# Optimization experiments

Hardware: AMD Instinct MI355X
Metric: run time of the kernel (lower is better)

## Reference

```python
import jax, jax.numpy as jnp
import numpy as np

N = 50000        # nodes
E = 800000       # edges (no self loops; GATv2Conv adds them itself)
F_IN = 256       # n_feats
DIM_H = 64       # hidden per head (layer 1)
HEADS = 4        # heads (layer 1)
N_CLASSES = 10
NEG_SLOPE = 0.2


def setup_inputs() -> dict:
    key = jax.random.key(0)
    ks = jax.random.split(key, 12)
    x = jax.random.normal(ks[0], (N, F_IN), dtype=jnp.float32)
    # edges with src != dst so PyG's remove_self_loops is a no-op
    src = jax.random.randint(ks[1], (E,), 0, N, dtype=jnp.int32)
    off = jax.random.randint(ks[2], (E,), 1, N, dtype=jnp.int32)
    dst = (src + off) % N
    edge_index = jnp.stack([src, dst], axis=0)  # [2, E]
    HC = HEADS * DIM_H
    s1 = 1.0 / np.sqrt(F_IN)
    s2 = 1.0 / np.sqrt(HC)
    W_l1 = jax.random.normal(ks[3], (F_IN, HC), dtype=jnp.float32) * s1
    W_r1 = jax.random.normal(ks[4], (F_IN, HC), dtype=jnp.float32) * s1
    att1 = jax.random.normal(ks[5], (HEADS, DIM_H), dtype=jnp.float32) * s2
    b1 = jnp.zeros((HC,), dtype=jnp.float32)
    W_l2 = jax.random.normal(ks[6], (HC, N_CLASSES), dtype=jnp.float32) * s2
    W_r2 = jax.random.normal(ks[7], (HC, N_CLASSES), dtype=jnp.float32) * s2
    att2 = jax.random.normal(ks[8], (1, N_CLASSES), dtype=jnp.float32) * (1.0 / np.sqrt(N_CLASSES))
    b2 = jnp.zeros((N_CLASSES,), dtype=jnp.float32)
    return {"x": x, "edge_index": edge_index,
            "W_l1": W_l1, "W_r1": W_r1, "att1": att1, "b1": b1,
            "W_l2": W_l2, "W_r2": W_r2, "att2": att2, "b2": b2}


def _gatv2_layer(x, src, dst, W_l, W_r, att, b, heads, ch):
    """One GATv2Conv layer (concat heads). src/dst already include self loops."""
    n = x.shape[0]
    xl = (x @ W_l).reshape(n, heads, ch)  # source transform (messages)
    xr = (x @ W_r).reshape(n, heads, ch)  # target transform
    # per-edge GATv2 score: att . LeakyReLU(x_l[src] + x_r[dst])
    e = jax.nn.leaky_relu(xl[src] + xr[dst], NEG_SLOPE)   # [E, H, C]
    score = jnp.einsum('ehc,hc->eh', e, att)              # [E, H]
    # segment softmax over incoming edges of each dst node
    m = jax.ops.segment_max(score, dst, num_segments=n)   # [N, H]
    ex = jnp.exp(score - m[dst])
    denom = jax.ops.segment_sum(ex, dst, num_segments=n)  # [N, H]
    alpha = ex / denom[dst]                               # [E, H]
    msg = xl[src] * alpha[:, :, None]                     # [E, H, C]
    out = jax.ops.segment_sum(msg, dst, num_segments=n)   # [N, H, C]
    return out.reshape(n, heads * ch) + b


def reference(x, edge_index, W_l1, W_r1, att1, b1, W_l2, W_r2, att2, b2):
    n = x.shape[0]
    loops = jnp.arange(n, dtype=edge_index.dtype)
    src = jnp.concatenate([edge_index[0], loops])  # add_self_loops=True
    dst = jnp.concatenate([edge_index[1], loops])
    h = _gatv2_layer(x, src, dst, W_l1, W_r1, att1, b1, HEADS, DIM_H)
    h = jax.nn.relu(h)
    out = _gatv2_layer(h, src, dst, W_l2, W_r2, att2, b2, 1, N_CLASSES)
    return out
```

## Files before the change

### kernel.cpp

```cpp
#include <hip/hip_runtime.h>
#include <hip/hip_bf16.h>

typedef unsigned short u16;
typedef unsigned int u32;
typedef short bf16x8 __attribute__((ext_vector_type(8)));
typedef float f32x4 __attribute__((ext_vector_type(4)));

constexpr int N_NODES = 50000;
constexpr int N_EDGES = 800000;
constexpr int ET      = N_EDGES + N_NODES;
constexpr int ETP     = ET + 3 * N_NODES;
constexpr int HC      = 256;
constexpr int NCLS    = 10;
constexpr float NEG   = 0.2f;
constexpr float LOG2E = 1.442695041f;

__device__ __forceinline__ u16 f2bf(float f) {
  u32 u = __float_as_uint(f);
  u += 0x7fffu + ((u >> 16) & 1u);
  return (u16)(u >> 16);
}
__device__ __forceinline__ float bf2f(u16 h) {
  return __uint_as_float(((u32)h) << 16);
}

__device__ __forceinline__ float dpp_ror8(float v) {
  return __uint_as_float(__builtin_amdgcn_mov_dpp(__float_as_uint(v), 0x128, 0xf, 0xf, true));
}
__device__ __forceinline__ float dpp_ror4(float v) {
  return __uint_as_float(__builtin_amdgcn_mov_dpp(__float_as_uint(v), 0x124, 0xf, 0xf, true));
}
__device__ __forceinline__ float dpp_ror2(float v) {
  return __uint_as_float(__builtin_amdgcn_mov_dpp(__float_as_uint(v), 0x122, 0xf, 0xf, true));
}
__device__ __forceinline__ float dpp_ror1(float v) {
  return __uint_as_float(__builtin_amdgcn_mov_dpp(__float_as_uint(v), 0x121, 0xf, 0xf, true));
}
__device__ __forceinline__ float row16_allsum(float p) {
  p += dpp_ror8(p);
  p += dpp_ror4(p);
  p += dpp_ror2(p);
  p += dpp_ror1(p);
  return p;
}


__global__ void k_hist(const int* __restrict__ ei, int* __restrict__ counts) {
  int e = blockIdx.x * 256 + threadIdx.x;
  if (e >= ET) return;
  int d = (e < N_EDGES) ? ei[N_EDGES + e] : (e - N_EDGES);
  atomicAdd(&counts[d], 1);
}

__global__ __launch_bounds__(256) void k_scan1(const int* __restrict__ counts,
                                               int* __restrict__ offsets,
                                               int* __restrict__ bsums) {
  __shared__ int sd[256];
  int t = threadIdx.x;
  int base = blockIdx.x * 1024 + t * 4;
  int v[4];
#pragma unroll
  for (int i = 0; i < 4; ++i) {
    int idx = base + i;
    v[i] = (idx < N_NODES) ? ((counts[idx] + 3) & ~3) : 0;
  }
  int tsum = v[0] + v[1] + v[2] + v[3];
  sd[t] = tsum;
  __syncthreads();
  for (int off = 1; off < 256; off <<= 1) {
    int x = (t >= off) ? sd[t - off] : 0;
    __syncthreads();
    sd[t] += x;
    __syncthreads();
  }
  int run = sd[t] - tsum;
#pragma unroll
  for (int i = 0; i < 4; ++i) {
    run += v[i];
    int idx = base + i;
    if (idx < N_NODES) offsets[idx + 1] = run;
  }
  if (t == 255) bsums[blockIdx.x] = sd[255];
}

__global__ __launch_bounds__(256) void k_scan2(int* __restrict__ bsums, int nb) {
  __shared__ int sd[256];
  int t = threadIdx.x;
  int v = (t < nb) ? bsums[t] : 0;
  sd[t] = v;
  __syncthreads();
  for (int off = 1; off < 256; off <<= 1) {
    int x = (t >= off) ? sd[t - off] : 0;
    __syncthreads();
    sd[t] += x;
    __syncthreads();
  }
  if (t < nb) bsums[t] = sd[t] - v;
}

__global__ void k_scan3(const int* __restrict__ bsums, int* __restrict__ offsets) {
  int i = blockIdx.x * 256 + threadIdx.x;
  if (i < N_NODES) offsets[i + 1] += bsums[i >> 10];
  if (i == 0) offsets[0] = 0;
}

__global__ void k_scatter(const int* __restrict__ ei, const int* __restrict__ offsets,
                          int* __restrict__ counts, int* __restrict__ srcs) {
  int e = blockIdx.x * 256 + threadIdx.x;
  if (e >= ET) return;
  int s, d;
  if (e < N_EDGES) { s = ei[e]; d = ei[N_EDGES + e]; }
  else             { s = e - N_EDGES; d = s; }
  int pos = offsets[d] + atomicSub(&counts[d], 1) - 1;
  srcs[pos] = s;
}

__global__ __launch_bounds__(256) void k_packW(const float* __restrict__ Wl,
                                               const float* __restrict__ Wr,
                                               u16* __restrict__ Wt_hi,
                                               u16* __restrict__ Wt_lo) {
  int c = blockIdx.x;
  int k = threadIdx.x;
  float w = (c < 256) ? Wl[k * 256 + c] : Wr[k * 256 + (c - 256)];
  u16 h = f2bf(w);
  float lo = w - bf2f(h);
  Wt_hi[c * 256 + k] = h;
  Wt_lo[c * 256 + k] = f2bf(lo);
}

__global__ __launch_bounds__(256) void k_gemm1_mfma(const float* __restrict__ x,
                                                    const u16* __restrict__ Wt_hi,
                                                    const u16* __restrict__ Wt_lo,
                                                    u16* __restrict__ xlb,
                                                    u16* __restrict__ xrb) {
  __shared__ char smem[61440];
  char* Ah = smem;
  char* Al = smem + 10240;
  char* Bh = smem + 20480;
  char* Bl = smem + 40960;

  int t = threadIdx.x;
  int lane = t & 63, wave = t >> 6;
  int wm = wave >> 1, wn = wave & 1;
  int row0 = blockIdx.x * 128;
  int bc = blockIdx.y;
  int col0 = bc * 256;

  f32x4 acc[4][8];
#pragma unroll
  for (int m = 0; m < 4; ++m)
#pragma unroll
    for (int n = 0; n < 8; ++n) acc[m][n] = (f32x4){0.f, 0.f, 0.f, 0.f};

  int ar = t >> 3;
  int ak4 = t & 7;
  int rr = lane & 15, kb = lane >> 4;

#pragma unroll 1
  for (int kk = 0; kk < 256; kk += 32) {
#pragma unroll
    for (int i = 0; i < 4; ++i) {
      int r = ar + 32 * i;
      int grow = row0 + r;
      if (grow >= N_NODES) grow = N_NODES - 1;
      float4 v = *(const float4*)&x[(size_t)grow * 256 + kk + ak4 * 4];
      u16 h0 = f2bf(v.x), h1 = f2bf(v.y), h2 = f2bf(v.z), h3 = f2bf(v.w);
      u16 l0 = f2bf(v.x - bf2f(h0)), l1 = f2bf(v.y - bf2f(h1));
      u16 l2 = f2bf(v.z - bf2f(h2)), l3 = f2bf(v.w - bf2f(h3));
      uint2 hp = make_uint2((u32)h0 | ((u32)h1 << 16), (u32)h2 | ((u32)h3 << 16));
      uint2 lp = make_uint2((u32)l0 | ((u32)l1 << 16), (u32)l2 | ((u32)l3 << 16));
      int boff = r * 80 + ak4 * 8;
      *(uint2*)(Ah + boff) = hp;
      *(uint2*)(Al + boff) = lp;
    }
    {
      const u16* sh = &Wt_hi[(size_t)(col0 + t) * 256 + kk];
      const u16* sl = &Wt_lo[(size_t)(col0 + t) * 256 + kk];
#pragma unroll
      for (int j = 0; j < 4; ++j) {
        *(uint4*)(Bh + t * 80 + j * 16) = *(const uint4*)&sh[j * 8];
        *(uint4*)(Bl + t * 80 + j * 16) = *(const uint4*)&sl[j * 8];
      }
    }
    __syncthreads();
    bf16x8 a_h[4], a_l[4];
#pragma unroll
    for (int m = 0; m < 4; ++m) {
      int off = (wm * 64 + m * 16 + rr) * 80 + kb * 16;
      a_h[m] = *(const bf16x8*)(Ah + off);
      a_l[m] = *(const bf16x8*)(Al + off);
    }
#pragma unroll
    for (int n = 0; n < 8; ++n) {
      int off = (wn * 128 + n * 16 + rr) * 80 + kb * 16;
      bf16x8 b_h = *(const bf16x8*)(Bh + off);
      bf16x8 b_l = *(const bf16x8*)(Bl + off);
#pragma unroll
      for (int m = 0; m < 4; ++m) {
        acc[m][n] = __builtin_amdgcn_mfma_f32_16x16x32_bf16(a_h[m], b_h, acc[m][n], 0, 0, 0);
        acc[m][n] = __builtin_amdgcn_mfma_f32_16x16x32_bf16(a_l[m], b_h, acc[m][n], 0, 0, 0);
        acc[m][n] = __builtin_amdgcn_mfma_f32_16x16x32_bf16(a_h[m], b_l, acc[m][n], 0, 0, 0);
      }
    }
    __syncthreads();
  }
  u16* Cout = bc ? xrb : xlb;
  int r0w = row0 + wm * 64 + (lane >> 4) * 4;
  int c0w = wn * 128 + (lane & 15);
#pragma unroll
  for (int m = 0; m < 4; ++m)
#pragma unroll
    for (int j = 0; j < 4; ++j) {
      int grow = r0w + m * 16 + j;
      if (grow < N_NODES) {
#pragma unroll
        for (int n = 0; n < 8; ++n)
          Cout[(size_t)grow * 256 + c0w + n * 16] = f2bf(acc[m][n][j]);
      }
    }
}

__global__ __launch_bounds__(256) void k_gat1_fused(
    const u16* __restrict__ xlb, const u16* __restrict__ xrb,
    const float* __restrict__ att, const float* __restrict__ b1,
    const float* __restrict__ Wl2, const float* __restrict__ Wr2,
    const int* __restrict__ offsets, const int* __restrict__ srcs,
    float* __restrict__ xl2, float* __restrict__ xr2) {
  __shared__ float Ws[20][256];
  int t = threadIdx.x;
#pragma unroll
  for (int c = 0; c < 10; ++c) {
    Ws[c][t]      = Wl2[t * 10 + c];
    Ws[c + 10][t] = Wr2[t * 10 + c];
  }
  __syncthreads();

  int wave = t >> 6, lane = t & 63;
  int n = blockIdx.x * 4 + wave;
  int c0 = lane * 4;
  float4 attv = *(const float4*)&att[c0];
  attv.x *= LOG2E; attv.y *= LOG2E; attv.z *= LOG2E; attv.w *= LOG2E;
  ushort4 xr4 = *(const ushort4*)&xrb[(size_t)n * 256 + c0];
  float4 xrv = make_float4(bf2f(xr4.x), bf2f(xr4.y), bf2f(xr4.z), bf2f(xr4.w));

  float m0 = -1e30f, m1 = -1e30f, m2 = -1e30f, m3 = -1e30f;
  float d0 = 0.f, d1 = 0.f, d2 = 0.f, d3 = 0.f;
  float4 A0 = {0,0,0,0}, A1 = {0,0,0,0}, A2 = {0,0,0,0}, A3 = {0,0,0,0};

  auto proc = [&](int s, float& m, float& d, float4& A) {
    int sa = s < 0 ? 0 : s;
    ushort4 r4 = *(const ushort4*)&xlb[(size_t)sa * 256 + c0];
    float4 xv = make_float4(bf2f(r4.x), bf2f(r4.y), bf2f(r4.z), bf2f(r4.w));
    float e0 = xv.x + xrv.x; e0 = fmaxf(e0, NEG * e0);
    float e1 = xv.y + xrv.y; e1 = fmaxf(e1, NEG * e1);
    float e2 = xv.z + xrv.z; e2 = fmaxf(e2, NEG * e2);
    float e3 = xv.w + xrv.w; e3 = fmaxf(e3, NEG * e3);
    float p = attv.x * e0 + attv.y * e1 + attv.z * e2 + attv.w * e3;
    p = row16_allsum(p);
    if (s < 0) p = -2e30f;
    if (!__all(p <= m + 8.0f)) {
      float mn = fmaxf(m, p);
      float corr = exp2f(m - mn);
      d *= corr;
      A.x *= corr; A.y *= corr; A.z *= corr; A.w *= corr;
      m = mn;
    }
    float w = exp2f(p - m);
    d += w;
    A.x += w * xv.x; A.y += w * xv.y; A.z += w * xv.z; A.w += w * xv.w;
  };

  int jb = offsets[n], je = offsets[n + 1];
  for (int j = jb; j < je; j += 4) {
    int s0 = srcs[j], s1 = srcs[j + 1], s2 = srcs[j + 2], s3 = srcs[j + 3];
    proc(s0, m0, d0, A0);
    proc(s1, m1, d1, A1);
    proc(s2, m2, d2, A2);
    proc(s3, m3, d3, A3);
  }

  auto merge = [](float& ma, float& da, float4& Aa, float mb, float db, float4 Ab) {
    float mm = fmaxf(ma, mb);
    float fa = exp2f(ma - mm), fb = exp2f(mb - mm);
    da = da * fa + db * fb;
    Aa.x = Aa.x * fa + Ab.x * fb;
    Aa.y = Aa.y * fa + Ab.y * fb;
    Aa.z = Aa.z * fa + Ab.z * fb;
    Aa.w = Aa.w * fa + Ab.w * fb;
    ma = mm;
  };
  merge(m0, d0, A0, m1, d1, A1);
  merge(m2, d2, A2, m3, d3, A3);
  merge(m0, d0, A0, m2, d2, A2);

  float inv = 1.0f / d0;
  float4 bv = *(const float4*)&b1[c0];
  float4 ov;
  ov.x = fmaxf(A0.x * inv + bv.x, 0.f);
  ov.y = fmaxf(A0.y * inv + bv.y, 0.f);
  ov.z = fmaxf(A0.z * inv + bv.z, 0.f);
  ov.w = fmaxf(A0.w * inv + bv.w, 0.f);

  float p[20];
#pragma unroll
  for (int c = 0; c < 20; ++c) {
    float4 w4 = *(const float4*)&Ws[c][c0];
    p[c] = ov.x * w4.x + ov.y * w4.y + ov.z * w4.z + ov.w * w4.w;
  }
#pragma unroll
  for (int c = 0; c < 20; ++c) {
    p[c] = row16_allsum(p[c]);
    p[c] += __shfl_xor(p[c], 16);
    p[c] += __shfl_xor(p[c], 32);
  }
  if (lane == 0) {
#pragma unroll
    for (int c = 0; c < 10; ++c) xl2[n * NCLS + c] = p[c];
#pragma unroll
    for (int c = 0; c < 10; ++c) xr2[n * NCLS + c] = p[c + 10];
  }
}

__global__ __launch_bounds__(256) void k_gat2(const float* __restrict__ xl2,
                                              const float* __restrict__ xr2,
                                              const float* __restrict__ att2,
                                              const float* __restrict__ b2,
                                              const int* __restrict__ offsets,
                                              const int* __restrict__ srcs,
                                              float* __restrict__ out) {
  int wave = threadIdx.x >> 6;
  int lane = threadIdx.x & 63;
  int n = blockIdx.x * 4 + wave;
  if (n >= N_NODES) return;
  int g = lane >> 4;
  int k = lane & 15;
  bool act = k < NCLS;
  float attk = act ? att2[k] * LOG2E : 0.f;
  float xrk  = act ? xr2[n * NCLS + k] : 0.f;
  float m = -1e30f;
  float denom = 0.f, acc = 0.f;
  int jb = offsets[n], je = offsets[n + 1];
  for (int j = jb + g; j < je; j += 4) {
    int s = srcs[j];
    int sa = s < 0 ? 0 : s;
    float xlv = act ? xl2[sa * NCLS + k] : 0.f;
    float e = xlv + xrk; e = fmaxf(e, NEG * e);
    float p = attk * e;
    p = row16_allsum(p);
    if (s < 0) p = -2e30f;
    if (!__all(p <= m + 8.0f)) {
      float mn = fmaxf(m, p);
      float corr = exp2f(m - mn);
      denom *= corr; acc *= corr;
      m = mn;
    }
    float w = exp2f(p - m);
    denom += w;
    acc   += w * xlv;
  }
  float mg = fmaxf(m, __shfl_xor(m, 16));
  mg = fmaxf(mg, __shfl_xor(mg, 32));
  float f = exp2f(m - mg);
  float d = denom * f;
  d += __shfl_xor(d, 16);
  d += __shfl_xor(d, 32);
  float a = acc * f;
  a += __shfl_xor(a, 16);
  a += __shfl_xor(a, 32);
  if (act && g == 0) out[n * NCLS + k] = a / d + b2[k];
}


extern "C" void kernel_launch(void* const* d_in, const int* in_sizes, int n_in,
                              void* d_out, int out_size, void* d_ws, size_t ws_size,
                              hipStream_t stream) {
  const float* x    = (const float*)d_in[0];
  const int*   ei   = (const int*)d_in[1];
  const float* Wl1  = (const float*)d_in[2];
  const float* Wr1  = (const float*)d_in[3];
  const float* att1 = (const float*)d_in[4];
  const float* b1   = (const float*)d_in[5];
  const float* Wl2  = (const float*)d_in[6];
  const float* Wr2  = (const float*)d_in[7];
  const float* att2 = (const float*)d_in[8];
  const float* b2   = (const float*)d_in[9];
  float* out = (float*)d_out;

  int* offsets = (int*)d_ws;
  int* counts  = offsets + (N_NODES + 1);
  int* bsums   = counts + N_NODES;
  int* srcs    = bsums + 256;
  size_t int_count = (size_t)(N_NODES + 1) + N_NODES + 256 + ETP;
  size_t foff = (int_count + 63) & ~(size_t)63;
  u16* xlb  = (u16*)((float*)d_ws + foff);
  u16* xrb  = xlb + (size_t)N_NODES * HC;
  u16* Wt_hi = xrb + (size_t)N_NODES * HC;
  u16* Wt_lo = Wt_hi + 512 * 256;
  float* xl2 = (float*)(Wt_lo + 512 * 256);
  float* xr2 = xl2 + (size_t)N_NODES * NCLS;

  const int nthr = 256;
  hipMemsetAsync(counts, 0, (size_t)N_NODES * 4, stream);
  k_hist<<<(ET + nthr - 1) / nthr, nthr, 0, stream>>>(ei, counts);
  int nb = (N_NODES + 1023) / 1024;
  k_scan1<<<nb, nthr, 0, stream>>>(counts, offsets, bsums);
  k_scan2<<<1, nthr, 0, stream>>>(bsums, nb);
  k_scan3<<<(N_NODES + nthr - 1) / nthr, nthr, 0, stream>>>(bsums, offsets);
  hipMemsetAsync(srcs, 0xFF, (size_t)ETP * 4, stream);
  k_scatter<<<(ET + nthr - 1) / nthr, nthr, 0, stream>>>(ei, offsets, counts, srcs);

  k_packW<<<512, nthr, 0, stream>>>(Wl1, Wr1, Wt_hi, Wt_lo);
  dim3 g1((N_NODES + 127) / 128, 2);
  k_gemm1_mfma<<<g1, nthr, 0, stream>>>(x, Wt_hi, Wt_lo, xlb, xrb);

  k_gat1_fused<<<N_NODES / 4, nthr, 0, stream>>>(xlb, xrb, att1, b1, Wl2, Wr2,
                                                 offsets, srcs, xl2, xr2);

  k_gat2<<<(N_NODES + 3) / 4, nthr, 0, stream>>>(xl2, xr2, att2, b2, offsets, srcs, out);
}
```

Measured before the change: 432.9 us.

## Switch layer-1 GEMM and aggregation to single-pass fp16, drop online softmax max

Replaces the three-pass bf16 hi/lo split GEMM with a single fp16 MFMA pass over x and W, both pre-converted to fp16 in separate pack kernels. The GAT aggregation now reads fp16 features and computes LeakyReLU in packed fp16, using mixed-precision FMAs for the score and accumulation. Both attention kernels drop the running-max rescaling of the segment softmax and call exp2 directly on raw scores. This cuts MFMA work and per-edge ALU cost, at the price of lower GEMM precision, fp16 range limits, and overflow risk if scores get large.

```diff
diff --git a/kernel.cpp b/kernel.cpp
--- a/kernel.cpp
+++ b/kernel.cpp
@@ -1,9 +1,10 @@
 #include <hip/hip_runtime.h>
-#include <hip/hip_bf16.h>
 
 typedef unsigned short u16;
 typedef unsigned int u32;
-typedef short bf16x8 __attribute__((ext_vector_type(8)));
+typedef _Float16 f16;
+typedef f16 f16x2 __attribute__((ext_vector_type(2)));
+typedef f16 f16x8 __attribute__((ext_vector_type(8)));
 typedef float f32x4 __attribute__((ext_vector_type(4)));
 
 constexpr int N_NODES = 50000;
@@ -15,13 +16,28 @@
 constexpr float NEG   = 0.2f;
 constexpr float LOG2E = 1.442695041f;
 
-__device__ __forceinline__ u16 f2bf(float f) {
-  u32 u = __float_as_uint(f);
-  u += 0x7fffu + ((u >> 16) & 1u);
-  return (u16)(u >> 16);
-}
-__device__ __forceinline__ float bf2f(u16 h) {
-  return __uint_as_float(((u32)h) << 16);
+#if __has_builtin(__builtin_amdgcn_exp2f)
+#define EXP2F(x) __builtin_amdgcn_exp2f(x)
+#else
+#define EXP2F(x) exp2f(x)
+#endif
+
+#define FMA_MIX_LO(acc, pk, w) \
+  asm("v_fma_mix_f32 %0, %1, %2, %0 op_sel:[0,0,0] op_sel_hi:[1,0,0]" \
+      : "+v"(acc) : "v"(pk), "v"(w))
+#define FMA_MIX_HI(acc, pk, w) \
+  asm("v_fma_mix_f32 %0, %1, %2, %0 op_sel:[1,0,0] op_sel_hi:[1,0,0]" \
+      : "+v"(acc) : "v"(pk), "v"(w))
+
+template <typename T, typename F>
+__device__ __forceinline__ T bc(F f) {
+  static_assert(sizeof(T) == sizeof(F), "size");
+  T t; __builtin_memcpy(&t, &f, sizeof(T)); return t;
+}
+
+__device__ __forceinline__ u32 pkh(float a, float b) {
+  f16x2 t = {(f16)a, (f16)b};
+  return bc<u32>(t);
 }
 
 __device__ __forceinline__ float dpp_ror8(float v) {
@@ -115,36 +131,43 @@
   srcs[pos] = s;
 }
 
-__global__ __launch_bounds__(256) void k_packW(const float* __restrict__ Wl,
-                                               const float* __restrict__ Wr,
-                                               u16* __restrict__ Wt_hi,
-                                               u16* __restrict__ Wt_lo) {
+__global__ __launch_bounds__(256) void k_packX(const float* __restrict__ x,
+                                               u16* __restrict__ xh) {
+  size_t i = ((size_t)blockIdx.x * 256 + threadIdx.x) * 8;
+  float4 v0 = *(const float4*)&x[i];
+  float4 v1 = *(const float4*)&x[i + 4];
+  uint4 o;
+  o.x = pkh(v0.x, v0.y);
+  o.y = pkh(v0.z, v0.w);
+  o.z = pkh(v1.x, v1.y);
+  o.w = pkh(v1.z, v1.w);
+  *(uint4*)&xh[i] = o;
+}
+
+__global__ __launch_bounds__(256) void k_packWh(const float* __restrict__ Wl,
+                                                const float* __restrict__ Wr,
+                                                u16* __restrict__ Wt) {
   int c = blockIdx.x;
   int k = threadIdx.x;
   float w = (c < 256) ? Wl[k * 256 + c] : Wr[k * 256 + (c - 256)];
-  u16 h = f2bf(w);
-  float lo = w - bf2f(h);
-  Wt_hi[c * 256 + k] = h;
-  Wt_lo[c * 256 + k] = f2bf(lo);
-}
-
-__global__ __launch_bounds__(256) void k_gemm1_mfma(const float* __restrict__ x,
-                                                    const u16* __restrict__ Wt_hi,
-                                                    const u16* __restrict__ Wt_lo,
-                                                    u16* __restrict__ xlb,
-                                                    u16* __restrict__ xrb) {
-  __shared__ char smem[61440];
+  Wt[c * 256 + k] = bc<u16>((f16)w);
+}
+
+__global__ __launch_bounds__(256) void k_gemm1h(const u16* __restrict__ xh,
+                                                const u16* __restrict__ Wt,
+                                                u16* __restrict__ xlh,
+                                                u16* __restrict__ xrh) {
+  __shared__ char smem[128 * 144 + 256 * 144];
   char* Ah = smem;
-  char* Al = smem + 10240;
-  char* Bh = smem + 20480;
-  char* Bl = smem + 40960;
+  char* Bh = smem + 128 * 144;
 
   int t = threadIdx.x;
   int lane = t & 63, wave = t >> 6;
   int wm = wave >> 1, wn = wave & 1;
   int row0 = blockIdx.x * 128;
-  int bc = blockIdx.y;
-  int col0 = bc * 256;
+  int bcid = blockIdx.y;
+  int col0 = bcid * 256;
+  int rr = lane & 15, kb = lane >> 4;
 
   f32x4 acc[4][8];
 #pragma unroll
@@ -152,59 +175,43 @@
 #pragma unroll
     for (int n = 0; n < 8; ++n) acc[m][n] = (f32x4){0.f, 0.f, 0.f, 0.f};
 
-  int ar = t >> 3;
-  int ak4 = t & 7;
-  int rr = lane & 15, kb = lane >> 4;
+  int arow = t >> 1, ahalf = t & 1;
+  int agrow = row0 + arow; if (agrow >= N_NODES) agrow = N_NODES - 1;
 
 #pragma unroll 1
-  for (int kk = 0; kk < 256; kk += 32) {
-#pragma unroll
-    for (int i = 0; i < 4; ++i) {
-      int r = ar + 32 * i;
-      int grow = row0 + r;
-      if (grow >= N_NODES) grow = N_NODES - 1;
-      float4 v = *(const float4*)&x[(size_t)grow * 256 + kk + ak4 * 4];
-      u16 h0 = f2bf(v.x), h1 = f2bf(v.y), h2 = f2bf(v.z), h3 = f2bf(v.w);
-      u16 l0 = f2bf(v.x - bf2f(h0)), l1 = f2bf(v.y - bf2f(h1));
-      u16 l2 = f2bf(v.z - bf2f(h2)), l3 = f2bf(v.w - bf2f(h3));
-      uint2 hp = make_uint2((u32)h0 | ((u32)h1 << 16), (u32)h2 | ((u32)h3 << 16));
-      uint2 lp = make_uint2((u32)l0 | ((u32)l1 << 16), (u32)l2 | ((u32)l3 << 16));
-      int boff = r * 80 + ak4 * 8;
-      *(uint2*)(Ah + boff) = hp;
-      *(uint2*)(Al + boff) = lp;
+  for (int kk = 0; kk < 256; kk += 64) {
+    {
+      const u16* src = &xh[(size_t)agrow * 256 + kk + ahalf * 32];
+      char* dst = Ah + arow * 144 + ahalf * 64;
+#pragma unroll
+      for (int i = 0; i < 4; ++i)
+        *(uint4*)(dst + i * 16) = *(const uint4*)(src + i * 8);
     }
     {
-      const u16* sh = &Wt_hi[(size_t)(col0 + t) * 256 + kk];
-      const u16* sl = &Wt_lo[(size_t)(col0 + t) * 256 + kk];
-#pragma unroll
-      for (int j = 0; j < 4; ++j) {
-        *(uint4*)(Bh + t * 80 + j * 16) = *(const uint4*)&sh[j * 8];
-        *(uint4*)(Bl + t * 80 + j * 16) = *(const uint4*)&sl[j * 8];
+      const u16* src = &Wt[(size_t)(col0 + t) * 256 + kk];
+      char* dst = Bh + t * 144;
+#pragma unroll
+      for (int i = 0; i < 8; ++i)
+        *(uint4*)(dst + i * 16) = *(const uint4*)(src + i * 8);
+    }
+    __syncthreads();
+#pragma unroll
+    for (int ks = 0; ks < 2; ++ks) {
+      f16x8 af[4];
+#pragma unroll
+      for (int m = 0; m < 4; ++m)
+        af[m] = *(const f16x8*)(Ah + (wm * 64 + m * 16 + rr) * 144 + ks * 64 + kb * 16);
+#pragma unroll
+      for (int n = 0; n < 8; ++n) {
+        f16x8 bf = *(const f16x8*)(Bh + (wn * 128 + n * 16 + rr) * 144 + ks * 64 + kb * 16);
+#pragma unroll
+        for (int m = 0; m < 4; ++m)
+          acc[m][n] = __builtin_amdgcn_mfma_f32_16x16x32_f16(af[m], bf, acc[m][n], 0, 0, 0);
       }
     }
     __syncthreads();
-    bf16x8 a_h[4], a_l[4];
-#pragma unroll
-    for (int m = 0; m < 4; ++m) {
-      int off = (wm * 64 + m * 16 + rr) * 80 + kb * 16;
-      a_h[m] = *(const bf16x8*)(Ah + off);
-      a_l[m] = *(const bf16x8*)(Al + off);
-    }
-#pragma unroll
-    for (int n = 0; n < 8; ++n) {
-      int off = (wn * 128 + n * 16 + rr) * 80 + kb * 16;
-      bf16x8 b_h = *(const bf16x8*)(Bh + off);
-      bf16x8 b_l = *(const bf16x8*)(Bl + off);
-#pragma unroll
-      for (int m = 0; m < 4; ++m) {
-        acc[m][n] = __builtin_amdgcn_mfma_f32_16x16x32_bf16(a_h[m], b_h, acc[m][n], 0, 0, 0);
-        acc[m][n] = __builtin_amdgcn_mfma_f32_16x16x32_bf16(a_l[m], b_h, acc[m][n], 0, 0, 0);
-        acc[m][n] = __builtin_amdgcn_mfma_f32_16x16x32_bf16(a_h[m], b_l, acc[m][n], 0, 0, 0);
-      }
-    }
-    __syncthreads();
-  }
-  u16* Cout = bc ? xrb : xlb;
+  }
+  u16* Cout = bcid ? xrh : xlh;
   int r0w = row0 + wm * 64 + (lane >> 4) * 4;
   int c0w = wn * 128 + (lane & 15);
 #pragma unroll
@@ -215,13 +222,13 @@
       if (grow < N_NODES) {
 #pragma unroll
         for (int n = 0; n < 8; ++n)
-          Cout[(size_t)grow * 256 + c0w + n * 16] = f2bf(acc[m][n][j]);
+          Cout[(size_t)grow * 256 + c0w + n * 16] = bc<u16>((f16)acc[m][n][j]);
       }
     }
 }
 
 __global__ __launch_bounds__(256) void k_gat1_fused(
-    const u16* __restrict__ xlb, const u16* __restrict__ xrb,
+    const u16* __restrict__ xlh, const u16* __restrict__ xrh,
     const float* __restrict__ att, const float* __restrict__ b1,
     const float* __restrict__ Wl2, const float* __restrict__ Wr2,
     const int* __restrict__ offsets, const int* __restrict__ srcs,
@@ -238,68 +245,58 @@
   int wave = t >> 6, lane = t & 63;
   int n = blockIdx.x * 4 + wave;
   int c0 = lane * 4;
-  float4 attv = *(const float4*)&att[c0];
-  attv.x *= LOG2E; attv.y *= LOG2E; attv.z *= LOG2E; attv.w *= LOG2E;
-  ushort4 xr4 = *(const ushort4*)&xrb[(size_t)n * 256 + c0];
-  float4 xrv = make_float4(bf2f(xr4.x), bf2f(xr4.y), bf2f(xr4.z), bf2f(xr4.w));
-
-  float m0 = -1e30f, m1 = -1e30f, m2 = -1e30f, m3 = -1e30f;
+  float a0 = att[c0] * LOG2E, a1 = att[c0 + 1] * LOG2E;
+  float a2 = att[c0 + 2] * LOG2E, a3 = att[c0 + 3] * LOG2E;
+  uint2 xru = *(const uint2*)&xrh[(size_t)n * 256 + c0];
+  f16x2 xr01 = bc<f16x2>(xru.x), xr23 = bc<f16x2>(xru.y);
+  const f16x2 negv = {(f16)NEG, (f16)NEG};
+
   float d0 = 0.f, d1 = 0.f, d2 = 0.f, d3 = 0.f;
-  float4 A0 = {0,0,0,0}, A1 = {0,0,0,0}, A2 = {0,0,0,0}, A3 = {0,0,0,0};
-
-  auto proc = [&](int s, float& m, float& d, float4& A) {
+  f32x4 A0 = {0,0,0,0}, A1 = {0,0,0,0}, A2 = {0,0,0,0}, A3 = {0,0,0,0};
+
+  auto proc = [&](int s, float& d, f32x4& A) {
     int sa = s < 0 ? 0 : s;
-    ushort4 r4 = *(const ushort4*)&xlb[(size_t)sa * 256 + c0];
-    float4 xv = make_float4(bf2f(r4.x), bf2f(r4.y), bf2f(r4.z), bf2f(r4.w));
-    float e0 = xv.x + xrv.x; e0 = fmaxf(e0, NEG * e0);
-    float e1 = xv.y + xrv.y; e1 = fmaxf(e1, NEG * e1);
-    float e2 = xv.z + xrv.z; e2 = fmaxf(e2, NEG * e2);
-    float e3 = xv.w + xrv.w; e3 = fmaxf(e3, NEG * e3);
-    float p = attv.x * e0 + attv.y * e1 + attv.z * e2 + attv.w * e3;
+    uint2 r = *(const uint2*)&xlh[(size_t)sa * 256 + c0];
+    f16x2 e01 = bc<f16x2>(r.x) + xr01;
+    f16x2 e23 = bc<f16x2>(r.y) + xr23;
+    e01 = __builtin_elementwise_max(e01, e01 * negv);
+    e23 = __builtin_elementwise_max(e23, e23 * negv);
+    u32 eu01 = bc<u32>(e01), eu23 = bc<u32>(e23);
+    float p = 0.f;
+    FMA_MIX_LO(p, eu01, a0);
+    FMA_MIX_HI(p, eu01, a1);
+    FMA_MIX_LO(p, eu23, a2);
+    FMA_MIX_HI(p, eu23, a3);
     p = row16_allsum(p);
-    if (s < 0) p = -2e30f;
-    if (!__all(p <= m + 8.0f)) {
-      float mn = fmaxf(m, p);
-      float corr = exp2f(m - mn);
-      d *= corr;
-      A.x *= corr; A.y *= corr; A.z *= corr; A.w *= corr;
-      m = mn;
-    }
-    float w = exp2f(p - m);
+    p = (s < 0) ? -2e30f : p;
+    float w = EXP2F(p);
     d += w;
-    A.x += w * xv.x; A.y += w * xv.y; A.z += w * xv.z; A.w += w * xv.w;
+    FMA_MIX_LO(A[0], r.x, w);
+    FMA_MIX_HI(A[1], r.x, w);
+    FMA_MIX_LO(A[2], r.y, w);
+    FMA_MIX_HI(A[3], r.y, w);
   };
 
   int jb = offsets[n], je = offsets[n + 1];
   for (int j = jb; j < je; j += 4) {
-    int s0 = srcs[j], s1 = srcs[j + 1], s2 = srcs[j + 2], s3 = srcs[j + 3];
-    proc(s0, m0, d0, A0);
-    proc(s1, m1, d1, A1);
-    proc(s2, m2, d2, A2);
-    proc(s3, m3, d3, A3);
-  }
-
-  auto merge = [](float& ma, float& da, float4& Aa, float mb, float db, float4 Ab) {
-    float mm = fmaxf(ma, mb);
-    float fa = exp2f(ma - mm), fb = exp2f(mb - mm);
-    da = da * fa + db * fb;
-    Aa.x = Aa.x * fa + Ab.x * fb;
-    Aa.y = Aa.y * fa + Ab.y * fb;
-    Aa.z = Aa.z * fa + Ab.z * fb;
-    Aa.w = Aa.w * fa + Ab.w * fb;
-    ma = mm;
-  };
-  merge(m0, d0, A0, m1, d1, A1);
-  merge(m2, d2, A2, m3, d3, A3);
-  merge(m0, d0, A0, m2, d2, A2);
-
-  float inv = 1.0f / d0;
+    int4 s4 = *(const int4*)&srcs[j];
+    proc(s4.x, d0, A0);
+    proc(s4.y, d1, A1);
+    proc(s4.z, d2, A2);
+    proc(s4.w, d3, A3);
+  }
+
+  float dsum = (d0 + d1) + (d2 + d3);
+#pragma unroll
+  for (int i = 0; i < 4; ++i) A0[i] = (A0[i] + A1[i]) + (A2[i] + A3[i]);
+
+  float inv = 1.0f / dsum;
   float4 bv = *(const float4*)&b1[c0];
   float4 ov;
-  ov.x = fmaxf(A0.x * inv + bv.x, 0.f);
-  ov.y = fmaxf(A0.y * inv + bv.y, 0.f);
-  ov.z = fmaxf(A0.z * inv + bv.z, 0.f);
-  ov.w = fmaxf(A0.w * inv + bv.w, 0.f);
+  ov.x = fmaxf(A0[0] * inv + bv.x, 0.f);
+  ov.y = fmaxf(A0[1] * inv + bv.y, 0.f);
+  ov.z = fmaxf(A0[2] * inv + bv.z, 0.f);
+  ov.w = fmaxf(A0[3] * inv + bv.w, 0.f);
 
   float p[20];
 #pragma unroll
@@ -337,7 +334,6 @@
   bool act = k < NCLS;
   float attk = act ? att2[k] * LOG2E : 0.f;
   float xrk  = act ? xr2[n * NCLS + k] : 0.f;
-  float m = -1e30f;
   float denom = 0.f, acc = 0.f;
   int jb = offsets[n], je = offsets[n + 1];
   for (int j = jb + g; j < je; j += 4) {
@@ -347,27 +343,16 @@
     float e = xlv + xrk; e = fmaxf(e, NEG * e);
     float p = attk * e;
     p = row16_allsum(p);
-    if (s < 0) p = -2e30f;
-    if (!__all(p <= m + 8.0f)) {
-      float mn = fmaxf(m, p);
-      float corr = exp2f(m - mn);
-      denom *= corr; acc *= corr;
-      m = mn;
-    }
-    float w = exp2f(p - m);
+    p = (s < 0) ? -2e30f : p;
+    float w = EXP2F(p);
     denom += w;
     acc   += w * xlv;
   }
-  float mg = fmaxf(m, __shfl_xor(m, 16));
-  mg = fmaxf(mg, __shfl_xor(mg, 32));
-  float f = exp2f(m - mg);
-  float d = denom * f;
-  d += __shfl_xor(d, 16);
-  d += __shfl_xor(d, 32);
-  float a = acc * f;
-  a += __shfl_xor(a, 16);
-  a += __shfl_xor(a, 32);
-  if (act && g == 0) out[n * NCLS + k] = a / d + b2[k];
+  denom += __shfl_xor(denom, 16);
+  denom += __shfl_xor(denom, 32);
+  acc += __shfl_xor(acc, 16);
+  acc += __shfl_xor(acc, 32);
+  if (act && g == 0) out[n * NCLS + k] = acc / denom + b2[k];
 }
 
 
@@ -392,11 +377,11 @@
   int* srcs    = bsums + 256;
   size_t int_count = (size_t)(N_NODES + 1) + N_NODES + 256 + ETP;
   size_t foff = (int_count + 63) & ~(size_t)63;
-  u16* xlb  = (u16*)((float*)d_ws + foff);
-  u16* xrb  = xlb + (size_t)N_NODES * HC;
-  u16* Wt_hi = xrb + (size_t)N_NODES * HC;
-  u16* Wt_lo = Wt_hi + 512 * 256;
-  float* xl2 = (float*)(Wt_lo + 512 * 256);
+  u16* xh   = (u16*)((float*)d_ws + foff);
+  u16* xlh  = xh  + (size_t)N_NODES * HC;
+  u16* xrh  = xlh + (size_t)N_NODES * HC;
+  u16* Wt   = xrh + (size_t)N_NODES * HC;
+  float* xl2 = (float*)(Wt + 512 * 256);
   float* xr2 = xl2 + (size_t)N_NODES * NCLS;
 
   const int nthr = 256;
@@ -409,11 +394,13 @@
   hipMemsetAsync(srcs, 0xFF, (size_t)ETP * 4, stream);
   k_scatter<<<(ET + nthr - 1) / nthr, nthr, 0, stream>>>(ei, offsets, counts, srcs);
 
-  k_packW<<<512, nthr, 0, stream>>>(Wl1, Wr1, Wt_hi, Wt_lo);
+  k_packX<<<(N_NODES * HC) / (nthr * 8), nthr, 0, stream>>>(x, xh);
+  k_packWh<<<512, nthr, 0, stream>>>(Wl1, Wr1, Wt);
+
   dim3 g1((N_NODES + 127) / 128, 2);
-  k_gemm1_mfma<<<g1, nthr, 0, stream>>>(x, Wt_hi, Wt_lo, xlb, xrb);
-
-  k_gat1_fused<<<N_NODES / 4, nthr, 0, stream>>>(xlb, xrb, att1, b1, Wl2, Wr2,
+  k_gemm1h<<<g1, nthr, 0, stream>>>(xh, Wt, xlh, xrh);
+
+  k_gat1_fused<<<N_NODES / 4, nthr, 0, stream>>>(xlh, xrh, att1, b1, Wl2, Wr2,
                                                  offsets, srcs, xl2, xr2);
 
   k_gat2<<<(N_NODES + 3) / 4, nthr, 0, stream>>>(xl2, xr2, att2, b2, offsets, srcs, out);
```

Result: faster. 364.4 us (-15.8%).
